# Kernel optimization log

Measured on AMD Instinct MI355X. Metric: run time of the kernel, lower is better.

The kernel has to match this reference:

```python
import jax, jax.numpy as jnp
import numpy as np

B, T, I, H, SEQLEN = 16384, 60, 32, 128, 30


def setup_inputs() -> dict:
    key = jax.random.key(0)
    ks = jax.random.split(key, 8)
    s_ih = 1.0 / np.sqrt(H)
    return {
        "x": jax.random.normal(ks[0], (B, T, I), dtype=jnp.float32),
        "h": jax.random.normal(ks[1], (1, B, H), dtype=jnp.float32),
        # GRU params (PyTorch layout: gates [r, z, n] stacked along dim 0)
        "W_ih": jax.random.uniform(ks[2], (3 * H, I), minval=-s_ih, maxval=s_ih, dtype=jnp.float32),
        "W_hh": jax.random.uniform(ks[3], (3 * H, H), minval=-s_ih, maxval=s_ih, dtype=jnp.float32),
        "b_ih": jax.random.uniform(ks[4], (3 * H,), minval=-s_ih, maxval=s_ih, dtype=jnp.float32),
        "b_hh": jax.random.uniform(ks[5], (3 * H,), minval=-s_ih, maxval=s_ih, dtype=jnp.float32),
        # output projection: hidden -> n_inputs
        "W_out": jax.random.uniform(ks[6], (I, H), minval=-s_ih, maxval=s_ih, dtype=jnp.float32),
        "b_out": jax.random.uniform(ks[7], (I,), minval=-s_ih, maxval=s_ih, dtype=jnp.float32),
    }


def _gru_cell(x_t, h, W_ih, W_hh, b_ih, b_hh):
    # x_t: [B, I], h: [B, H]
    gi = x_t @ W_ih.T + b_ih          # [B, 3H]
    gh = h @ W_hh.T + b_hh            # [B, 3H]
    i_r, i_z, i_n = jnp.split(gi, 3, axis=-1)
    h_r, h_z, h_n = jnp.split(gh, 3, axis=-1)
    r = jax.nn.sigmoid(i_r + h_r)
    z = jax.nn.sigmoid(i_z + h_z)
    n = jnp.tanh(i_n + r * h_n)
    return (1.0 - z) * n + z * h


def reference(x, h, W_ih, W_hh, b_ih, b_hh, W_out, b_out):
    xout = x[:, SEQLEN:, :]            # [B, steps, I]
    steps = xout.shape[1]
    h0 = h[0]                          # single layer, unidirectional -> [B, H]
    x0 = xout[:, 0, :]                 # [B, I]

    def step(carry, _):
        x_t, h_t = carry
        h_new = _gru_cell(x_t, h_t, W_ih, W_hh, b_ih, b_hh)
        y = h_new @ W_out.T + b_out    # [B, I], fed back as next input
        return (y, h_new), y

    _, ys = jax.lax.scan(step, (x0, h0), None, length=steps)  # ys: [steps, B, I]
    return jnp.transpose(ys, (1, 0, 2))                        # [B, steps, I]
```

## Files before the change

kernel.cpp:

```cpp
#include <hip/hip_runtime.h>


#define NB    16384
#define TT    60
#define II    32
#define HH    128
#define NSTEP 30
#define SEQ0  30
#define BM    64
#define HBS   136
#define XBS   40

#define WS_WSTAR 0
#define WS_BSTAR (384 * 128)

typedef __attribute__((ext_vector_type(8))) short bf16x8;
typedef __attribute__((ext_vector_type(4))) float f32x4;

#define MFMA(a, b, c) __builtin_amdgcn_mfma_f32_16x16x32_bf16((a), (b), (c), 0, 0, 0)

__device__ __forceinline__ short f2bf(float x) {
    unsigned u = __float_as_uint(x);
    u += 0x7FFFu + ((u >> 16) & 1u);
    return (short)(u >> 16);
}
__device__ __forceinline__ bf16x8 ldw8(const float* p) {
    float4 a = *(const float4*)p;
    float4 b = *(const float4*)(p + 4);
    bf16x8 f;
    f[0] = f2bf(a.x); f[1] = f2bf(a.y); f[2] = f2bf(a.z); f[3] = f2bf(a.w);
    f[4] = f2bf(b.x); f[5] = f2bf(b.y); f[6] = f2bf(b.z); f[7] = f2bf(b.w);
    return f;
}
__device__ __forceinline__ float sigm(float a) {
    return __builtin_amdgcn_rcpf(1.0f + __expf(-a));
}
__device__ __forceinline__ float tanh_(float a) {
    return 1.0f - 2.0f * __builtin_amdgcn_rcpf(1.0f + __expf(2.0f * a));
}

__global__ void fold_kernel(const float* __restrict__ Wih,
                            const float* __restrict__ Whh,
                            const float* __restrict__ bih,
                            const float* __restrict__ bhh,
                            const float* __restrict__ Wout,
                            const float* __restrict__ bout,
                            float* __restrict__ ws)
{
    const int jg = blockIdx.x;
    const int k  = threadIdx.x;
    const int gate = jg >> 7;
    float acc  = (gate < 2) ? Whh[(size_t)jg * HH + k] : 0.0f;
    float bacc = 0.0f;
    #pragma unroll 8
    for (int i = 0; i < II; ++i) {
        const float w = Wih[(size_t)jg * II + i];
        acc  += w * Wout[(size_t)i * HH + k];
        bacc += w * bout[i];
    }
    ws[WS_WSTAR + (size_t)jg * HH + k] = acc;
    if (k == 0)
        ws[WS_BSTAR + jg] = bih[jg] + ((gate < 2) ? bhh[jg] : 0.0f) + bacc;
}

__global__ __launch_bounds__(512, 2)
void gru_mfma_kernel(const float* __restrict__ x,
                     const float* __restrict__ h0,
                     const float* __restrict__ Wih,
                     const float* __restrict__ Whh,
                     const float* __restrict__ bih,
                     const float* __restrict__ bhh,
                     const float* __restrict__ Wout,
                     const float* __restrict__ bout,
                     const float* __restrict__ ws,
                     float* __restrict__ out)
{
    __shared__ short shb[2][BM * HBS];
    __shared__ short sxb[BM * XBS];

    const int tid    = threadIdx.x;
    const int lane   = tid & 63;
    const int wave   = __builtin_amdgcn_readfirstlane(tid >> 6);
    const int n16    = lane & 15;
    const int quad   = lane >> 4;
    const int rowblk = blockIdx.x * BM;
    const int j      = wave * 16 + n16;

    bf16x8 Bnh[4];
    float  b_nh;
    {
        const float* wn = Whh + (size_t)(2 * HH + j) * HH;
        #pragma unroll
        for (int kt = 0; kt < 4; ++kt)
            Bnh[kt] = ldw8(wn + kt * 32 + quad * 8);
        b_nh = bhh[2 * HH + j];
    }
    const int rowtile = wave >> 1;
    const int coltile = wave & 1;
    bf16x8 Bo[4];
    float  b_o;
    {
        const int i = coltile * 16 + n16;
        #pragma unroll
        for (int kt = 0; kt < 4; ++kt)
            Bo[kt] = ldw8(Wout + (size_t)i * HH + kt * 32 + quad * 8);
        b_o = bout[i];
    }

    float hst[4][4];
    #pragma unroll
    for (int mt = 0; mt < 4; ++mt)
        #pragma unroll
        for (int reg = 0; reg < 4; ++reg)
            hst[mt][reg] = h0[(size_t)(rowblk + mt * 16 + quad * 4 + reg) * HH + j];

    {
        const int r  = tid >> 3;
        const int c0 = (tid & 7) * 16;
        const float* src = h0 + (size_t)(rowblk + r) * HH + c0;
        *(bf16x8*)&shb[0][r * HBS + c0]     = ldw8(src);
        *(bf16x8*)&shb[0][r * HBS + c0 + 8] = ldw8(src + 8);
    }
    if (tid < 256) {
        const int r  = tid >> 2;
        const int c0 = (tid & 3) * 8;
        const float* src = x + ((size_t)(rowblk + r) * TT + SEQ0) * II + c0;
        *(bf16x8*)&sxb[r * XBS + c0] = ldw8(src);
    }
    __syncthreads();

    {
        bf16x8 Br0[4], Bz0[4], Bxr, Bxz, Bxn;
        const float* wr = Whh + (size_t)j * HH;
        const float* wz = Whh + (size_t)(HH + j) * HH;
        #pragma unroll
        for (int kt = 0; kt < 4; ++kt) {
            Br0[kt] = ldw8(wr + kt * 32 + quad * 8);
            Bz0[kt] = ldw8(wz + kt * 32 + quad * 8);
        }
        Bxr = ldw8(Wih + (size_t)j * II + quad * 8);
        Bxz = ldw8(Wih + (size_t)(HH + j) * II + quad * 8);
        Bxn = ldw8(Wih + (size_t)(2 * HH + j) * II + quad * 8);
        const float b_r0 = bih[j] + bhh[j];
        const float b_z0 = bih[HH + j] + bhh[HH + j];
        const float b_n0 = bih[2 * HH + j];

        #pragma unroll
        for (int mt = 0; mt < 4; ++mt) {
            bf16x8 A[4], Ax;
            #pragma unroll
            for (int kt = 0; kt < 4; ++kt)
                A[kt] = *(const bf16x8*)&shb[0][(mt * 16 + n16) * HBS + kt * 32 + quad * 8];
            Ax = *(const bf16x8*)&sxb[(mt * 16 + n16) * XBS + quad * 8];

            f32x4 ar  = (f32x4){b_r0, b_r0, b_r0, b_r0};
            f32x4 az  = (f32x4){b_z0, b_z0, b_z0, b_z0};
            f32x4 anh = (f32x4){b_nh, b_nh, b_nh, b_nh};
            f32x4 anx = (f32x4){b_n0, b_n0, b_n0, b_n0};
            #pragma unroll
            for (int kt = 0; kt < 4; ++kt) {
                ar  = MFMA(A[kt], Br0[kt], ar);
                az  = MFMA(A[kt], Bz0[kt], az);
                anh = MFMA(A[kt], Bnh[kt], anh);
            }
            ar  = MFMA(Ax, Bxr, ar);
            az  = MFMA(Ax, Bxz, az);
            anx = MFMA(Ax, Bxn, anx);

            #pragma unroll
            for (int reg = 0; reg < 4; ++reg) {
                const float r = sigm(ar[reg]);
                const float z = sigm(az[reg]);
                const float n = tanh_(anx[reg] + r * anh[reg]);
                const float hnew = n + z * (hst[mt][reg] - n);
                hst[mt][reg] = hnew;
                shb[1][(mt * 16 + quad * 4 + reg) * HBS + j] = f2bf(hnew);
            }
        }
    }

    bf16x8 Brs[4], Bzs[4], Bni[4];
    float  b_rs, b_zs, b_ni;
    {
        const float* pr = ws + WS_WSTAR + (size_t)j * HH;
        const float* pz = ws + WS_WSTAR + (size_t)(HH + j) * HH;
        const float* pn = ws + WS_WSTAR + (size_t)(2 * HH + j) * HH;
        #pragma unroll
        for (int kt = 0; kt < 4; ++kt) {
            Brs[kt] = ldw8(pr + kt * 32 + quad * 8);
            Bzs[kt] = ldw8(pz + kt * 32 + quad * 8);
            Bni[kt] = ldw8(pn + kt * 32 + quad * 8);
        }
        b_rs = ws[WS_BSTAR + j];
        b_zs = ws[WS_BSTAR + HH + j];
        b_ni = ws[WS_BSTAR + 2 * HH + j];
    }

    __syncthreads();

    int p = 0;
    for (int s = 0; s < NSTEP; ++s) {
        const int q = 1 - p;

        {
            bf16x8 A2[4];
            #pragma unroll
            for (int kt = 0; kt < 4; ++kt)
                A2[kt] = *(const bf16x8*)&shb[q][(rowtile * 16 + n16) * HBS + kt * 32 + quad * 8];
            f32x4 yo = (f32x4){b_o, b_o, b_o, b_o};
            #pragma unroll
            for (int kt = 0; kt < 4; ++kt)
                yo = MFMA(A2[kt], Bo[kt], yo);
            #pragma unroll
            for (int reg = 0; reg < 4; ++reg) {
                const int r_l = rowtile * 16 + quad * 4 + reg;
                out[(size_t)(rowblk + r_l) * (NSTEP * II) + s * II + coltile * 16 + n16] = yo[reg];
            }
        }

        if (s == NSTEP - 1) break;

        #pragma unroll
        for (int mt = 0; mt < 4; ++mt) {
            bf16x8 A[4];
            #pragma unroll
            for (int kt = 0; kt < 4; ++kt)
                A[kt] = *(const bf16x8*)&shb[q][(mt * 16 + n16) * HBS + kt * 32 + quad * 8];

            f32x4 ar  = (f32x4){b_rs, b_rs, b_rs, b_rs};
            f32x4 az  = (f32x4){b_zs, b_zs, b_zs, b_zs};
            f32x4 anh = (f32x4){b_nh, b_nh, b_nh, b_nh};
            f32x4 ani = (f32x4){b_ni, b_ni, b_ni, b_ni};
            #pragma unroll
            for (int kt = 0; kt < 4; ++kt) {
                ar  = MFMA(A[kt], Brs[kt], ar);
                az  = MFMA(A[kt], Bzs[kt], az);
                anh = MFMA(A[kt], Bnh[kt], anh);
                ani = MFMA(A[kt], Bni[kt], ani);
            }

            #pragma unroll
            for (int reg = 0; reg < 4; ++reg) {
                const float r = sigm(ar[reg]);
                const float z = sigm(az[reg]);
                const float n = tanh_(ani[reg] + r * anh[reg]);
                const float hnew = n + z * (hst[mt][reg] - n);
                hst[mt][reg] = hnew;
                shb[p][(mt * 16 + quad * 4 + reg) * HBS + j] = f2bf(hnew);
            }
        }

        p = q;
        __syncthreads();
    }
}

extern "C" void kernel_launch(void* const* d_in, const int* in_sizes, int n_in,
                              void* d_out, int out_size, void* d_ws, size_t ws_size,
                              hipStream_t stream) {
    (void)in_sizes; (void)n_in; (void)out_size; (void)ws_size;
    const float* x    = (const float*)d_in[0];
    const float* h0   = (const float*)d_in[1];
    const float* Wih  = (const float*)d_in[2];
    const float* Whh  = (const float*)d_in[3];
    const float* bih  = (const float*)d_in[4];
    const float* bhh  = (const float*)d_in[5];
    const float* Wout = (const float*)d_in[6];
    const float* bout = (const float*)d_in[7];
    float* out = (float*)d_out;
    float* ws  = (float*)d_ws;

    fold_kernel<<<dim3(384), dim3(128), 0, stream>>>(Wih, Whh, bih, bhh,
                                                     Wout, bout, ws);
    dim3 grid(NB / BM);
    dim3 block(512);
    gru_mfma_kernel<<<grid, block, 0, stream>>>(x, h0, Wih, Whh, bih, bhh,
                                                Wout, bout, ws, out);
}
```

Before: 268.5 us.

## Halve batch tile per block, move W_out fragments to LDS, raise occupancy

Cuts the rows per block from 64 to 32, doubling the number of blocks, and raises the launch bound to 4 blocks per SM. W_out fragments now live in LDS instead of registers, and A fragments are loaded per k-tile instead of being held as whole arrays, all to lower VGPR pressure. The output projection now runs on only 4 waves. Each block does less work per barrier, so more blocks and waves can hide the serial recurrence latency. In exchange, the recurrent weight fragments are loaded once per block, so there are twice as many such loads, plus some extra LDS traffic.

```diff
diff --git a/kernel.cpp b/kernel.cpp
--- a/kernel.cpp
+++ b/kernel.cpp
@@ -7,8 +7,8 @@
 #define HH    128
 #define NSTEP 30
 #define SEQ0  30
-#define BM    64
-#define HBS   136
+#define BM    32
+#define HBS   144
 #define XBS   40
 
 #define WS_WSTAR 0
@@ -63,7 +63,7 @@
         ws[WS_BSTAR + jg] = bih[jg] + ((gate < 2) ? bhh[jg] : 0.0f) + bacc;
 }
 
-__global__ __launch_bounds__(512, 2)
+__global__ __launch_bounds__(512, 4)
 void gru_mfma_kernel(const float* __restrict__ x,
                      const float* __restrict__ h0,
                      const float* __restrict__ Wih,
@@ -77,6 +77,7 @@
 {
     __shared__ short shb[2][BM * HBS];
     __shared__ short sxb[BM * XBS];
+    __shared__ short sWo[2 * 4 * 64 * 8];
 
     const int tid    = threadIdx.x;
     const int lane   = tid & 63;
@@ -97,35 +98,32 @@
     }
     const int rowtile = wave >> 1;
     const int coltile = wave & 1;
-    bf16x8 Bo[4];
-    float  b_o;
-    {
-        const int i = coltile * 16 + n16;
-        #pragma unroll
-        for (int kt = 0; kt < 4; ++kt)
-            Bo[kt] = ldw8(Wout + (size_t)i * HH + kt * 32 + quad * 8);
-        b_o = bout[i];
-    }
-
-    float hst[4][4];
+    float b_o = 0.0f;
+    if (wave < 2) {
+        #pragma unroll
+        for (int kt = 0; kt < 4; ++kt) {
+            bf16x8 t = ldw8(Wout + (size_t)(wave * 16 + n16) * HH + kt * 32 + quad * 8);
+            *(bf16x8*)&sWo[((wave * 4 + kt) * 64 + lane) * 8] = t;
+        }
+    }
+    if (wave < 4) b_o = bout[coltile * 16 + n16];
+
+    float hst[2][4];
     #pragma unroll
-    for (int mt = 0; mt < 4; ++mt)
+    for (int mt = 0; mt < 2; ++mt)
         #pragma unroll
         for (int reg = 0; reg < 4; ++reg)
             hst[mt][reg] = h0[(size_t)(rowblk + mt * 16 + quad * 4 + reg) * HH + j];
 
     {
-        const int r  = tid >> 3;
-        const int c0 = (tid & 7) * 16;
-        const float* src = h0 + (size_t)(rowblk + r) * HH + c0;
-        *(bf16x8*)&shb[0][r * HBS + c0]     = ldw8(src);
-        *(bf16x8*)&shb[0][r * HBS + c0 + 8] = ldw8(src + 8);
-    }
-    if (tid < 256) {
+        const int r  = tid >> 4;
+        const int c0 = (tid & 15) * 8;
+        *(bf16x8*)&shb[0][r * HBS + c0] = ldw8(h0 + (size_t)(rowblk + r) * HH + c0);
+    }
+    if (tid < 128) {
         const int r  = tid >> 2;
         const int c0 = (tid & 3) * 8;
-        const float* src = x + ((size_t)(rowblk + r) * TT + SEQ0) * II + c0;
-        *(bf16x8*)&sxb[r * XBS + c0] = ldw8(src);
+        *(bf16x8*)&sxb[r * XBS + c0] = ldw8(x + ((size_t)(rowblk + r) * TT + SEQ0) * II + c0);
     }
     __syncthreads();
 
@@ -146,27 +144,24 @@
         const float b_n0 = bih[2 * HH + j];
 
         #pragma unroll
-        for (int mt = 0; mt < 4; ++mt) {
-            bf16x8 A[4], Ax;
-            #pragma unroll
-            for (int kt = 0; kt < 4; ++kt)
-                A[kt] = *(const bf16x8*)&shb[0][(mt * 16 + n16) * HBS + kt * 32 + quad * 8];
-            Ax = *(const bf16x8*)&sxb[(mt * 16 + n16) * XBS + quad * 8];
-
+        for (int mt = 0; mt < 2; ++mt) {
             f32x4 ar  = (f32x4){b_r0, b_r0, b_r0, b_r0};
             f32x4 az  = (f32x4){b_z0, b_z0, b_z0, b_z0};
             f32x4 anh = (f32x4){b_nh, b_nh, b_nh, b_nh};
             f32x4 anx = (f32x4){b_n0, b_n0, b_n0, b_n0};
             #pragma unroll
             for (int kt = 0; kt < 4; ++kt) {
-                ar  = MFMA(A[kt], Br0[kt], ar);
-                az  = MFMA(A[kt], Bz0[kt], az);
-                anh = MFMA(A[kt], Bnh[kt], anh);
-            }
-            ar  = MFMA(Ax, Bxr, ar);
-            az  = MFMA(Ax, Bxz, az);
-            anx = MFMA(Ax, Bxn, anx);
-
+                bf16x8 A = *(const bf16x8*)&shb[0][(mt * 16 + n16) * HBS + kt * 32 + quad * 8];
+                ar  = MFMA(A, Br0[kt], ar);
+                az  = MFMA(A, Bz0[kt], az);
+                anh = MFMA(A, Bnh[kt], anh);
+            }
+            {
+                bf16x8 Ax = *(const bf16x8*)&sxb[(mt * 16 + n16) * XBS + quad * 8];
+                ar  = MFMA(Ax, Bxr, ar);
+                az  = MFMA(Ax, Bxz, az);
+                anx = MFMA(Ax, Bxn, anx);
+            }
             #pragma unroll
             for (int reg = 0; reg < 4; ++reg) {
                 const float r = sigm(ar[reg]);
@@ -202,15 +197,14 @@
     for (int s = 0; s < NSTEP; ++s) {
         const int q = 1 - p;
 
-        {
-            bf16x8 A2[4];
-            #pragma unroll
-            for (int kt = 0; kt < 4; ++kt)
-                A2[kt] = *(const bf16x8*)&shb[q][(rowtile * 16 + n16) * HBS + kt * 32 + quad * 8];
+        if (wave < 4) {
             f32x4 yo = (f32x4){b_o, b_o, b_o, b_o};
             #pragma unroll
-            for (int kt = 0; kt < 4; ++kt)
-                yo = MFMA(A2[kt], Bo[kt], yo);
+            for (int kt = 0; kt < 4; ++kt) {
+                bf16x8 A2  = *(const bf16x8*)&shb[q][(rowtile * 16 + n16) * HBS + kt * 32 + quad * 8];
+                bf16x8 Bof = *(const bf16x8*)&sWo[((coltile * 4 + kt) * 64 + lane) * 8];
+                yo = MFMA(A2, Bof, yo);
+            }
             #pragma unroll
             for (int reg = 0; reg < 4; ++reg) {
                 const int r_l = rowtile * 16 + quad * 4 + reg;
@@ -221,24 +215,19 @@
         if (s == NSTEP - 1) break;
 
         #pragma unroll
-        for (int mt = 0; mt < 4; ++mt) {
-            bf16x8 A[4];
-            #pragma unroll
-            for (int kt = 0; kt < 4; ++kt)
-                A[kt] = *(const bf16x8*)&shb[q][(mt * 16 + n16) * HBS + kt * 32 + quad * 8];
-
+        for (int mt = 0; mt < 2; ++mt) {
             f32x4 ar  = (f32x4){b_rs, b_rs, b_rs, b_rs};
             f32x4 az  = (f32x4){b_zs, b_zs, b_zs, b_zs};
             f32x4 anh = (f32x4){b_nh, b_nh, b_nh, b_nh};
             f32x4 ani = (f32x4){b_ni, b_ni, b_ni, b_ni};
             #pragma unroll
             for (int kt = 0; kt < 4; ++kt) {
-                ar  = MFMA(A[kt], Brs[kt], ar);
-                az  = MFMA(A[kt], Bzs[kt], az);
-                anh = MFMA(A[kt], Bnh[kt], anh);
-                ani = MFMA(A[kt], Bni[kt], ani);
-            }
-
+                bf16x8 A = *(const bf16x8*)&shb[q][(mt * 16 + n16) * HBS + kt * 32 + quad * 8];
+                ar  = MFMA(A, Brs[kt], ar);
+                az  = MFMA(A, Bzs[kt], az);
+                anh = MFMA(A, Bnh[kt], anh);
+                ani = MFMA(A, Bni[kt], ani);
+            }
             #pragma unroll
             for (int reg = 0; reg < 4; ++reg) {
                 const float r = sigm(ar[reg]);
```

Result: slower. 283.9 us (+5.7%).
